# Performance work log

Measured on AMD Instinct MI355X. Metric: run time of the kernel, lower is better.

## Reference

```python
import jax, jax.numpy as jnp
import numpy as np

B, DV, W, H = 64, 2048, 14, 14
DQ, DA, G, DH, NC = 2400, 1200, 2, 1200, 3000


def setup_inputs() -> dict:
    key = jax.random.key(0)
    ks = jax.random.split(key, 14)
    s = lambda k, shp, scale=0.02: jax.random.normal(k, shp, dtype=jnp.float32) * scale
    return {
        "input_q": jax.random.normal(ks[0], (B, DQ), dtype=jnp.float32),
        "input_v": jax.random.normal(ks[1], (B, DV, W, H), dtype=jnp.float32),
        "Wv_att": s(ks[2], (DA, DV)),
        "bv_att": s(ks[3], (DA,)),
        "Wq_att": s(ks[4], (DA, DQ)),
        "bq_att": s(ks[5], (DA,)),
        "Watt": s(ks[6], (G, DA)),
        "batt": s(ks[7], (G,)),
        "Wv_fus": s(ks[8], (G, DH, DV)),
        "bv_fus": s(ks[9], (G, DH)),
        "Wq_fus": s(ks[10], (G * DH, DQ)),
        "bq_fus": s(ks[11], (G * DH,)),
        "Wc": s(ks[12], (NC, G * DH)),
        "bc": s(ks[13], (NC,)),
    }


def reference(input_q, input_v, Wv_att, bv_att, Wq_att, bq_att, Watt, batt,
              Wv_fus, bv_fus, Wq_fus, bq_fus, Wc, bc):
    b, dv, w, h = input_v.shape
    n = w * h  # spatial positions

    # --- attention branch (eval mode: dropout = identity) ---
    # 1x1 conv == per-position linear over channels; activation_v = tanh
    xv = jnp.tanh(jnp.einsum('bchw,dc->bdhw', input_v, Wv_att) + bv_att[None, :, None, None])
    xv = xv.reshape(b, -1, n).transpose(0, 2, 1)               # [B, WH, DA]
    # question projection; activation_q = tanh
    xq = jnp.tanh(input_q @ Wq_att.T + bq_att)                 # [B, DA]
    # MLB Hadamard fusion + activation_mm = tanh
    xatt = jnp.tanh(xv * xq[:, None, :])                       # [B, WH, DA]
    # glimpse scores: 1x1 conv over dim_mm channels
    wgt = jnp.einsum('bnd,gd->bgn', xatt, Watt) + batt[None, :, None]  # [B, G, WH]
    att = jax.nn.softmax(wgt, axis=-1)                         # softmax over WH per glimpse

    # weighted sum of ORIGINAL features per glimpse
    v_flat = input_v.reshape(b, dv, n)                         # [B, DV, WH]
    v_att = jnp.einsum('bgn,bdn->bgd', att, v_flat)            # [B, G, DV]

    # --- glimpse fusion + classification ---
    v_fus = jnp.tanh(jnp.einsum('bgd,ghd->bgh', v_att, Wv_fus) + bv_fus)  # [B, G, DH]
    v_fus = v_fus.reshape(b, -1)                               # [B, G*DH] (concat over glimpses)
    q_fus = jnp.tanh(input_q @ Wq_fus.T + bq_fus)              # [B, G*DH]
    x = (v_fus * q_fus) @ Wc.T + bc                            # [B, NC]
    return (x, wgt)
```

## Files before the change

kernel.cpp:

```cpp
#include <hip/hip_runtime.h>
#include <hip/hip_fp16.h>

typedef _Float16 half8 __attribute__((ext_vector_type(8)));
typedef float f32x4 __attribute__((ext_vector_type(4)));

__device__ __forceinline__ float tanh_fast(float x) {
  float e = __expf(2.0f * x);
  return 1.0f - 2.0f / (e + 1.0f);
}

__device__ __forceinline__ void gload16(const _Float16* g, _Float16* l) {
  __builtin_amdgcn_global_load_lds((const __attribute__((address_space(1))) void*)g,
                                   (__attribute__((address_space(3))) void*)l,
                                   16, 0, 0);
}

__global__ __launch_bounds__(256) void k_transpose_v(const float* __restrict__ in,
                                                     _Float16* __restrict__ out) {
  __shared__ float t[64][65];
  int b = blockIdx.z;
  int c0 = blockIdx.y * 64;
  int p0 = blockIdx.x * 64;
  int tid = threadIdx.x;
  int pl = tid & 63;
  #pragma unroll
  for (int s = 0; s < 16; ++s) {
    int cl = (tid >> 6) + s * 4;
    int p = p0 + pl;
    t[cl][pl] = (p < 196) ? in[((size_t)b * 2048 + (c0 + cl)) * 196 + p] : 0.0f;
  }
  __syncthreads();
  int c8 = (tid & 7) * 8;
  #pragma unroll
  for (int s = 0; s < 2; ++s) {
    int p = p0 + (tid >> 3) + s * 32;
    if (p < 196) {
      half8 v;
      #pragma unroll
      for (int j = 0; j < 8; ++j) v[j] = (_Float16)t[c8 + j][(tid >> 3) + s * 32];
      *(half8*)(out + ((size_t)b * 196 + p) * 2048 + c0 + c8) = v;
    }
  }
}

__global__ __launch_bounds__(256) void k_prep(const float* __restrict__ W,
                                              _Float16* __restrict__ Wh,
                                              const float* __restrict__ batt,
                                              float* __restrict__ wgt) {
  int i = blockIdx.x * 256 + threadIdx.x;
  int n = i >> 11;
  Wh[i] = (n < 1200) ? (_Float16)W[i] : (_Float16)0.0f;
  if (i < 25088) wgt[i] = batt[(i / 196) & 1];
}

__global__ __launch_bounds__(512, 2) void k_gemm1(const _Float16* __restrict__ A,
                                                  const _Float16* __restrict__ B,
                                                  const float* __restrict__ bias,
                                                  const float* __restrict__ xq,
                                                  const float* __restrict__ Watt,
                                                  float* __restrict__ wgt) {
  __shared__ __align__(16) _Float16 AS[2][256 * 64];
  __shared__ __align__(16) _Float16 BS[2][256 * 64];
  int tid = threadIdx.x;
  int lin = blockIdx.y * 5 + blockIdx.x;
  int xcd = lin & 7;
  int loc = lin >> 3;
  int nw = (xcd < 5 ? xcd * 31 : 155 + (xcd - 5) * 30) + loc;
  int n0 = (nw % 5) * 256;
  int m0 = (nw / 5) * 256;
  int lane = tid & 63;
  int wave = tid >> 6;
  int wm = (wave >> 2) * 128;
  int wn = (wave & 3) * 64;
  int fr = lane & 15;
  int fq = lane >> 4;

  int aIdx[2], bIdx[2];
  #pragma unroll
  for (int kk = 0; kk < 2; ++kk) {
    int sw = (((kk * 4 + fq) ^ (fr & 7)) << 3);
    aIdx[kk] = (wm + fr) * 64 + sw;
    bIdx[kk] = (wn + fr) * 64 + sw;
  }

  int lr = lane >> 3;
  int swz8 = ((lane & 7) ^ lr) << 3;
  const _Float16* aSrc[2][2];
  const _Float16* bSrc[2][2];
  int aDst[2][2], bDst[2][2];
  #pragma unroll
  for (int h = 0; h < 2; ++h)
    #pragma unroll
    for (int j = 0; j < 2; ++j) {
      int ra = j * 128 + h * 64 + wave * 8;
      aSrc[h][j] = A + (size_t)(m0 + ra + lr) * 2048 + swz8;
      aDst[h][j] = ra * 64;
      int rb = (j * 2 + (wave >> 2)) * 64 + h * 32 + (wave & 3) * 8;
      bSrc[h][j] = B + (size_t)(n0 + rb + lr) * 2048 + swz8;
      bDst[h][j] = rb * 64;
    }

  f32x4 acc[8][4];
  #pragma unroll
  for (int i = 0; i < 8; ++i)
    #pragma unroll
    for (int j = 0; j < 4; ++j) acc[i][j] = (f32x4){0.f, 0.f, 0.f, 0.f};

  auto stA = [&](int buf, int h, int off) {
    gload16(aSrc[h][0] + off, &AS[buf][aDst[h][0]]);
    gload16(aSrc[h][1] + off, &AS[buf][aDst[h][1]]);
  };
  auto stB = [&](int buf, int h, int off) {
    gload16(bSrc[h][0] + off, &BS[buf][bDst[h][0]]);
    gload16(bSrc[h][1] + off, &BS[buf][bDst[h][1]]);
  };
  auto dsA = [&](int buf, int mh, half8 (&a)[4][2]) {
    #pragma unroll
    for (int mt = 0; mt < 4; ++mt)
      #pragma unroll
      for (int kk = 0; kk < 2; ++kk)
        a[mt][kk] = *(const half8*)&AS[0][aIdx[kk] + (buf * 16384 + mh * 4096 + mt * 1024)];
  };
  auto dsB = [&](int buf, int nh, half8 (&b)[2][2]) {
    #pragma unroll
    for (int nt = 0; nt < 2; ++nt)
      #pragma unroll
      for (int kk = 0; kk < 2; ++kk)
        b[nt][kk] = *(const half8*)&BS[0][bIdx[kk] + (buf * 16384 + nh * 2048 + nt * 1024)];
  };
  auto mma = [&](half8 (&a)[4][2], half8 (&b)[2][2], int mh, int nh) {
    __builtin_amdgcn_s_setprio(1);
    #pragma unroll
    for (int kk = 0; kk < 2; ++kk)
      #pragma unroll
      for (int mt = 0; mt < 4; ++mt)
        #pragma unroll
        for (int nt = 0; nt < 2; ++nt)
          acc[mh * 4 + mt][nh * 2 + nt] = __builtin_amdgcn_mfma_f32_16x16x32_f16(
              a[mt][kk], b[nt][kk], acc[mh * 4 + mt][nh * 2 + nt], 0, 0, 0);
    __builtin_amdgcn_s_setprio(0);
  };

#define BAR() __builtin_amdgcn_s_barrier()
#define FENCE() asm volatile("" ::: "memory")
#define LGKM0() asm volatile("s_waitcnt lgkmcnt(0)")
#define LGKM8() asm volatile("s_waitcnt lgkmcnt(8)")

  stA(0, 0, 0); stB(0, 0, 0); stB(0, 1, 0); stA(0, 1, 0);
  stA(1, 0, 64); stB(1, 0, 64); stB(1, 1, 64);
  asm volatile("s_waitcnt vmcnt(6)" ::: "memory");
  BAR();
  FENCE();

  half8 a[4][2], b0[2][2], b1[2][2];
  for (int i = 0; i < 16; ++i) {
    const bool nl = (i < 15);
    dsA(0, 0, a); dsB(0, 0, b0);
    stA(1, 1, 64);
    LGKM8();
    BAR(); LGKM0();
    mma(a, b0, 0, 0);
    BAR();
    dsB(0, 1, b1);
    if (nl) stA(0, 0, 128);
    BAR(); LGKM0();
    mma(a, b1, 0, 1);
    BAR();
    dsA(0, 1, a);
    if (nl) stB(0, 0, 128);
    BAR(); LGKM0();
    mma(a, b1, 1, 1);
    BAR();
    if (nl) {
      stB(0, 1, 128);
      asm volatile("s_waitcnt vmcnt(6)" ::: "memory");
    } else {
      asm volatile("s_waitcnt vmcnt(0)" ::: "memory");
    }
    BAR();
    FENCE();
    mma(a, b0, 1, 0);
    BAR();
    dsA(1, 0, a); dsB(1, 0, b0);
    if (nl) stA(0, 1, 128);
    LGKM8();
    BAR(); LGKM0();
    mma(a, b0, 0, 0);
    BAR();
    dsB(1, 1, b1);
    if (nl) stA(1, 0, 192);
    BAR(); LGKM0();
    mma(a, b1, 0, 1);
    BAR();
    dsA(1, 1, a);
    if (nl) stB(1, 0, 192);
    BAR(); LGKM0();
    mma(a, b1, 1, 1);
    BAR();
    if (nl) {
      stB(1, 1, 192);
      asm volatile("s_waitcnt vmcnt(6)" ::: "memory");
    }
    BAR();
    FENCE();
    mma(a, b0, 1, 0);
    BAR();
    #pragma unroll
    for (int h = 0; h < 2; ++h)
      #pragma unroll
      for (int j = 0; j < 2; ++j) { aSrc[h][j] += 128; bSrc[h][j] += 128; }
  }
#undef BAR
#undef FENCE
#undef LGKM0
#undef LGKM8

  float bcol[4], wa0c[4], wa1c[4], xqv[4];
  int colv[4]; bool okv[4];
  #pragma unroll
  for (int nf = 0; nf < 4; ++nf) {
    int col = n0 + wn + (nf >> 1) * 32 + (nf & 1) * 16 + fr;
    bool ok = col < 1200;
    colv[nf] = col; okv[nf] = ok;
    bcol[nf] = ok ? bias[col] : 0.f;
    wa0c[nf] = ok ? Watt[col] : 0.f;
    wa1c[nf] = ok ? Watt[1200 + col] : 0.f;
    xqv[nf] = 0.f;
  }
  int bprev = -1;
  #pragma unroll
  for (int mf = 0; mf < 8; ++mf) {
    #pragma unroll
    for (int r = 0; r < 4; ++r) {
      int row = m0 + wm + (mf >> 2) * 64 + (mf & 3) * 16 + fq * 4 + r;
      int b = row / 196;
      if (b != bprev) {
        bprev = b;
        #pragma unroll
        for (int nf = 0; nf < 4; ++nf)
          xqv[nf] = okv[nf] ? xq[b * 1200 + colv[nf]] : 0.f;
      }
      float t0 = 0.f, t1 = 0.f;
      #pragma unroll
      for (int nf = 0; nf < 4; ++nf) {
        float xv = tanh_fast(acc[mf][nf][r] + bcol[nf]);
        float xa = tanh_fast(xv * xqv[nf]);
        t0 += xa * wa0c[nf];
        t1 += xa * wa1c[nf];
      }
      #pragma unroll
      for (int off = 8; off > 0; off >>= 1) {
        t0 += __shfl_down(t0, off);
        t1 += __shfl_down(t1, off);
      }
      if (fr == 0) {
        int p = row - b * 196;
        atomicAdd(&wgt[(b * 2 + 0) * 196 + p], t0);
        atomicAdd(&wgt[(b * 2 + 1) * 196 + p], t1);
      }
    }
  }
}

__global__ __launch_bounds__(512) void k_vatt(const _Float16* __restrict__ Vt,
                                              const float* __restrict__ wgt,
                                              float* __restrict__ v_att) {
  __shared__ float a0s[196], a1s[196];
  __shared__ float red[2][3][128][9];
  int b = blockIdx.y;
  int tid = threadIdx.x;
  int wv = tid >> 6, lane = tid & 63;
  if (wv < 2) {
    const float* wr = wgt + ((size_t)b * 2 + wv) * 196;
    float v[4];
    #pragma unroll
    for (int i = 0; i < 4; ++i) {
      int n = lane + i * 64;
      v[i] = (n < 196) ? wr[n] : -1e30f;
    }
    float mx = fmaxf(fmaxf(v[0], v[1]), fmaxf(v[2], v[3]));
    #pragma unroll
    for (int off = 32; off > 0; off >>= 1) mx = fmaxf(mx, __shfl_xor(mx, off));
    float s = 0.f;
    #pragma unroll
    for (int i = 0; i < 4; ++i) {
      int n = lane + i * 64;
      float e = (n < 196) ? __expf(v[i] - mx) : 0.f;
      v[i] = e;
      s += e;
    }
    #pragma unroll
    for (int off = 32; off > 0; off >>= 1) s += __shfl_xor(s, off);
    float inv = 1.f / s;
    float* dst = wv ? a1s : a0s;
    #pragma unroll
    for (int i = 0; i < 4; ++i) {
      int n = lane + i * 64;
      if (n < 196) dst[n] = v[i] * inv;
    }
  }
  __syncthreads();
  int nc = tid >> 7;
  int dl = tid & 127;
  int d = blockIdx.x * 1024 + dl * 8;
  const _Float16* vp = Vt + (size_t)b * 196 * 2048 + d;
  float s0[8] = {}, s1[8] = {};
  for (int n = nc * 49; n < nc * 49 + 49; ++n) {
    half8 v = *(const half8*)(vp + (size_t)n * 2048);
    float a0 = a0s[n], a1 = a1s[n];
    #pragma unroll
    for (int j = 0; j < 8; ++j) {
      float f = (float)v[j];
      s0[j] += a0 * f;
      s1[j] += a1 * f;
    }
  }
  if (nc > 0) {
    #pragma unroll
    for (int j = 0; j < 8; ++j) {
      red[0][nc - 1][dl][j] = s0[j];
      red[1][nc - 1][dl][j] = s1[j];
    }
  }
  __syncthreads();
  if (nc == 0) {
    #pragma unroll
    for (int c = 0; c < 3; ++c)
      #pragma unroll
      for (int j = 0; j < 8; ++j) {
        s0[j] += red[0][c][dl][j];
        s1[j] += red[1][c][dl][j];
      }
    #pragma unroll
    for (int j = 0; j < 8; ++j) {
      v_att[((size_t)b * 2 + 0) * 2048 + d + j] = s0[j];
      v_att[((size_t)b * 2 + 1) * 2048 + d + j] = s1[j];
    }
  }
}

__global__ __launch_bounds__(256) void k_skinnyQ(const float* __restrict__ q,
                                                 const float* __restrict__ Wa,
                                                 const float* __restrict__ Wf,
                                                 int S, float* __restrict__ P) {
  __shared__ __align__(16) float As[32][64];
  __shared__ __align__(16) float Ws2[32][64];
  int tid = threadIdx.x;
  int x = blockIdx.x;
  int s = blockIdx.y;
  bool f = x >= 19;
  const float* W = f ? Wf : Wa;
  int nt0 = f ? (x - 19) * 64 : x * 64;
  int N = f ? 2400 : 1200;
  int colBase = f ? 1200 : 0;
  const int K = 2400;
  int tiles = K >> 5;
  int t0 = (s * tiles) / S;
  int t1 = ((s + 1) * tiles) / S;
  int tx = tid & 15, ty = tid >> 4;
  int lm = tid >> 2;
  int lk = (tid & 3) * 8;
  const float* Ab = q + (size_t)lm * K;
  int ng = nt0 + lm;
  const float* Wb = W + (size_t)ng * K;
  bool wok = ng < N;
  float acc[4][4] = {};
  for (int t = t0; t < t1; ++t) {
    int k0 = t * 32;
    __syncthreads();
    #pragma unroll
    for (int j = 0; j < 8; ++j) As[lk + j][lm] = Ab[k0 + lk + j];
    #pragma unroll
    for (int j = 0; j < 8; ++j) Ws2[lk + j][lm] = wok ? Wb[k0 + lk + j] : 0.0f;
    __syncthreads();
    #pragma unroll
    for (int kk = 0; kk < 32; ++kk) {
      f32x4 a = *(const f32x4*)&As[kk][ty * 4];
      f32x4 wv = *(const f32x4*)&Ws2[kk][tx * 4];
      #pragma unroll
      for (int i = 0; i < 4; ++i)
        #pragma unroll
        for (int j = 0; j < 4; ++j) acc[i][j] += a[i] * wv[j];
    }
  }
  #pragma unroll
  for (int i = 0; i < 4; ++i) {
    int m = ty * 4 + i;
    #pragma unroll
    for (int j = 0; j < 4; ++j) {
      int nl = nt0 + tx * 4 + j;
      if (nl < N) P[((size_t)s * 64 + m) * 3600 + colBase + nl] = acc[i][j];
    }
  }
}

__global__ __launch_bounds__(256) void k_combineQ(const float* __restrict__ P, int S,
                                                  const float* __restrict__ bq_att,
                                                  const float* __restrict__ bq_fus,
                                                  float* __restrict__ xq,
                                                  float* __restrict__ q_fus) {
  int i = blockIdx.x * 256 + threadIdx.x;
  if (i >= 230400) return;
  int row = i / 3600, col = i % 3600;
  float sum = 0.f;
  for (int ss = 0; ss < S; ++ss) sum += P[(size_t)ss * 230400 + i];
  if (col < 1200) xq[row * 1200 + col] = tanh_fast(sum + bq_att[col]);
  else            q_fus[row * 2400 + col - 1200] = tanh_fast(sum + bq_fus[col - 1200]);
}

__global__ __launch_bounds__(256) void k_skinny(const float* __restrict__ A1,
                                                const float* __restrict__ A2,
                                                int lda, int strideAz,
                                                const float* __restrict__ W, long strideWz,
                                                int N, int K, int S,
                                                float* __restrict__ P, int ldp, int colOffZ) {
  __shared__ __align__(16) float As[32][64];
  __shared__ __align__(16) float Ws2[32][64];
  int tid = threadIdx.x;
  int z = blockIdx.z;
  int s = blockIdx.y;
  int nt0 = blockIdx.x * 64;
  int tiles = K >> 5;
  int t0 = (s * tiles) / S;
  int t1 = ((s + 1) * tiles) / S;
  int tx = tid & 15, ty = tid >> 4;
  int lm = tid >> 2;
  int lk = (tid & 3) * 8;
  const float* Ab = A1 + (size_t)z * strideAz + (size_t)lm * lda;
  const float* A2b = A2 ? (A2 + (size_t)z * strideAz + (size_t)lm * lda) : nullptr;
  int ng = nt0 + lm;
  const float* Wb = W + (size_t)z * strideWz + (size_t)ng * K;
  bool wok = ng < N;
  float acc[4][4] = {};
  for (int t = t0; t < t1; ++t) {
    int k0 = t * 32;
    __syncthreads();
    #pragma unroll
    for (int j = 0; j < 8; ++j) {
      float v = Ab[k0 + lk + j];
      if (A2b) v *= A2b[k0 + lk + j];
      As[lk + j][lm] = v;
    }
    #pragma unroll
    for (int j = 0; j < 8; ++j) Ws2[lk + j][lm] = wok ? Wb[k0 + lk + j] : 0.0f;
    __syncthreads();
    #pragma unroll
    for (int kk = 0; kk < 32; ++kk) {
      f32x4 a = *(const f32x4*)&As[kk][ty * 4];
      f32x4 wv = *(const f32x4*)&Ws2[kk][tx * 4];
      #pragma unroll
      for (int i = 0; i < 4; ++i)
        #pragma unroll
        for (int j = 0; j < 4; ++j) acc[i][j] += a[i] * wv[j];
    }
  }
  #pragma unroll
  for (int i = 0; i < 4; ++i) {
    int m = ty * 4 + i;
    #pragma unroll
    for (int j = 0; j < 4; ++j) {
      int nl = nt0 + tx * 4 + j;
      if (nl < N) P[((size_t)s * 64 + m) * ldp + z * colOffZ + nl] = acc[i][j];
    }
  }
}

__global__ __launch_bounds__(256) void k_combineVh(const float* __restrict__ P, int S,
                                                   const float* __restrict__ bv_fus,
                                                   const float* __restrict__ q_fus,
                                                   float* __restrict__ h) {
  int i = blockIdx.x * 256 + threadIdx.x;
  if (i >= 153600) return;
  int col = i % 2400;
  float sum = bv_fus[col];
  for (int ss = 0; ss < S; ++ss) sum += P[(size_t)ss * 153600 + i];
  h[i] = tanh_fast(sum) * q_fus[i];
}

__global__ __launch_bounds__(256) void k_combine(const float* __restrict__ P, int S, int ldp,
                                                 const float* __restrict__ bias,
                                                 float* __restrict__ out, int total) {
  int i = blockIdx.x * 256 + threadIdx.x;
  if (i >= total) return;
  float sum = bias[i % ldp];
  for (int ss = 0; ss < S; ++ss) sum += P[(size_t)ss * total + i];
  out[i] = sum;
}

extern "C" void kernel_launch(void* const* d_in, const int* in_sizes, int n_in,
                              void* d_out, int out_size, void* d_ws, size_t ws_size,
                              hipStream_t stream) {
  const float* input_q = (const float*)d_in[0];
  const float* input_v = (const float*)d_in[1];
  const float* Wv_att  = (const float*)d_in[2];
  const float* bv_att  = (const float*)d_in[3];
  const float* Wq_att  = (const float*)d_in[4];
  const float* bq_att  = (const float*)d_in[5];
  const float* Watt    = (const float*)d_in[6];
  const float* batt    = (const float*)d_in[7];
  const float* Wv_fus  = (const float*)d_in[8];
  const float* bv_fus  = (const float*)d_in[9];
  const float* Wq_fus  = (const float*)d_in[10];
  const float* bq_fus  = (const float*)d_in[11];
  const float* Wc      = (const float*)d_in[12];
  const float* bc      = (const float*)d_in[13];
  float* out = (float*)d_out;

  char* ws = (char*)d_ws;
  _Float16* Vt   = (_Float16*)ws; ws += 51380224;
  _Float16* Wh   = (_Float16*)ws; ws += 5242880;
  float* xq      = (float*)ws;    ws += 307200;
  float* v_att   = (float*)ws;    ws += 1048576;
  float* v_fus   = (float*)ws;    ws += 614400;
  float* q_fus   = (float*)ws;    ws += 614400;
  float* P       = (float*)ws;    ws += 14745600;

  float* x_out   = out;
  float* wgt_out = out + 192000;

  const int S = 16;

  k_transpose_v<<<dim3(4, 32, 64), dim3(256), 0, stream>>>(input_v, Vt);
  k_prep<<<dim3(10240), dim3(256), 0, stream>>>(Wv_att, Wh, batt, wgt_out);

  k_skinnyQ<<<dim3(57, S), dim3(256), 0, stream>>>(input_q, Wq_att, Wq_fus, S, P);
  k_combineQ<<<dim3(900), dim3(256), 0, stream>>>(P, S, bq_att, bq_fus, xq, q_fus);

  k_gemm1<<<dim3(5, 49), dim3(512), 0, stream>>>(Vt, Wh, bv_att, xq, Watt, wgt_out);

  k_vatt<<<dim3(2, 64), dim3(512), 0, stream>>>(Vt, wgt_out, v_att);

  k_skinny<<<dim3(19, S, 2), dim3(256), 0, stream>>>(v_att, nullptr, 4096, 2048,
                                                     Wv_fus, 1200L * 2048L, 1200, 2048, S, P, 2400, 1200);
  k_combineVh<<<dim3(600), dim3(256), 0, stream>>>(P, S, bv_fus, q_fus, v_fus);

  k_skinny<<<dim3(47, S, 1), dim3(256), 0, stream>>>(v_fus, nullptr, 2400, 0,
                                                     Wc, 0, 3000, 2400, S, P, 3000, 0);
  k_combine<<<dim3(750), dim3(256), 0, stream>>>(P, S, 3000, bc, x_out, 192000);
}
```

Baseline: 448.4 us.

## Drop explicit LDS waits in GEMM pipeline and repartition v_att kernel

The GEMM main loop loses its hand-placed lgkmcnt waits and about half its barriers, so the compiler inserts the LDS-read waits itself and MFMA work can overlap with LDS loads. The order of the LDS fragment loads is also swapped. Separately, the attention-weighted sum kernel now runs 256 threads per block over 8x64 blocks, each covering 256 channels with 8 spatial chunks instead of 4. This gives more blocks and more parallelism across spatial positions. With fewer barriers there is a risk of LDS buffer overwrite races if the remaining barriers no longer fully protect buffer reuse.

```diff
diff --git a/kernel.cpp b/kernel.cpp
--- a/kernel.cpp
+++ b/kernel.cpp
@@ -116,16 +116,16 @@
   };
   auto dsA = [&](int buf, int mh, half8 (&a)[4][2]) {
     #pragma unroll
-    for (int mt = 0; mt < 4; ++mt)
-      #pragma unroll
-      for (int kk = 0; kk < 2; ++kk)
+    for (int kk = 0; kk < 2; ++kk)
+      #pragma unroll
+      for (int mt = 0; mt < 4; ++mt)
         a[mt][kk] = *(const half8*)&AS[0][aIdx[kk] + (buf * 16384 + mh * 4096 + mt * 1024)];
   };
   auto dsB = [&](int buf, int nh, half8 (&b)[2][2]) {
     #pragma unroll
-    for (int nt = 0; nt < 2; ++nt)
-      #pragma unroll
-      for (int kk = 0; kk < 2; ++kk)
+    for (int kk = 0; kk < 2; ++kk)
+      #pragma unroll
+      for (int nt = 0; nt < 2; ++nt)
         b[nt][kk] = *(const half8*)&BS[0][bIdx[kk] + (buf * 16384 + nh * 2048 + nt * 1024)];
   };
   auto mma = [&](half8 (&a)[4][2], half8 (&b)[2][2], int mh, int nh) {
@@ -143,8 +143,6 @@
 
 #define BAR() __builtin_amdgcn_s_barrier()
 #define FENCE() asm volatile("" ::: "memory")
-#define LGKM0() asm volatile("s_waitcnt lgkmcnt(0)")
-#define LGKM8() asm volatile("s_waitcnt lgkmcnt(8)")
 
   stA(0, 0, 0); stB(0, 0, 0); stB(0, 1, 0); stA(0, 1, 0);
   stA(1, 0, 64); stB(1, 0, 64); stB(1, 1, 64);
@@ -155,56 +153,44 @@
   half8 a[4][2], b0[2][2], b1[2][2];
   for (int i = 0; i < 16; ++i) {
     const bool nl = (i < 15);
-    dsA(0, 0, a); dsB(0, 0, b0);
+    dsB(0, 0, b0); dsA(0, 0, a);
     stA(1, 1, 64);
-    LGKM8();
-    BAR(); LGKM0();
     mma(a, b0, 0, 0);
-    BAR();
+    BAR(); FENCE();
     dsB(0, 1, b1);
     if (nl) stA(0, 0, 128);
-    BAR(); LGKM0();
     mma(a, b1, 0, 1);
-    BAR();
+    BAR(); FENCE();
     dsA(0, 1, a);
     if (nl) stB(0, 0, 128);
-    BAR(); LGKM0();
     mma(a, b1, 1, 1);
-    BAR();
+    BAR(); FENCE();
     if (nl) {
       stB(0, 1, 128);
       asm volatile("s_waitcnt vmcnt(6)" ::: "memory");
     } else {
       asm volatile("s_waitcnt vmcnt(0)" ::: "memory");
     }
-    BAR();
-    FENCE();
     mma(a, b0, 1, 0);
-    BAR();
-    dsA(1, 0, a); dsB(1, 0, b0);
+    BAR(); FENCE();
+    dsB(1, 0, b0); dsA(1, 0, a);
     if (nl) stA(0, 1, 128);
-    LGKM8();
-    BAR(); LGKM0();
     mma(a, b0, 0, 0);
-    BAR();
+    BAR(); FENCE();
     dsB(1, 1, b1);
     if (nl) stA(1, 0, 192);
-    BAR(); LGKM0();
     mma(a, b1, 0, 1);
-    BAR();
+    BAR(); FENCE();
     dsA(1, 1, a);
     if (nl) stB(1, 0, 192);
-    BAR(); LGKM0();
     mma(a, b1, 1, 1);
-    BAR();
+    BAR(); FENCE();
     if (nl) {
       stB(1, 1, 192);
       asm volatile("s_waitcnt vmcnt(6)" ::: "memory");
     }
-    BAR();
-    FENCE();
     mma(a, b0, 1, 0);
-    BAR();
+    BAR(); FENCE();
     #pragma unroll
     for (int h = 0; h < 2; ++h)
       #pragma unroll
@@ -212,8 +198,6 @@
   }
 #undef BAR
 #undef FENCE
-#undef LGKM0
-#undef LGKM8
 
   float bcol[4], wa0c[4], wa1c[4], xqv[4];
   int colv[4]; bool okv[4];
@@ -262,11 +246,11 @@
   }
 }
 
-__global__ __launch_bounds__(512) void k_vatt(const _Float16* __restrict__ Vt,
+__global__ __launch_bounds__(256) void k_vatt(const _Float16* __restrict__ Vt,
                                               const float* __restrict__ wgt,
                                               float* __restrict__ v_att) {
   __shared__ float a0s[196], a1s[196];
-  __shared__ float red[2][3][128][9];
+  __shared__ float red[2][7][32][9];
   int b = blockIdx.y;
   int tid = threadIdx.x;
   int wv = tid >> 6, lane = tid & 63;
@@ -300,12 +284,13 @@
     }
   }
   __syncthreads();
-  int nc = tid >> 7;
-  int dl = tid & 127;
-  int d = blockIdx.x * 1024 + dl * 8;
+  int dg = tid & 31;
+  int nc = tid >> 5;
+  int d = blockIdx.x * 256 + dg * 8;
   const _Float16* vp = Vt + (size_t)b * 196 * 2048 + d;
+  int nA = (nc * 196) >> 3, nB = ((nc + 1) * 196) >> 3;
   float s0[8] = {}, s1[8] = {};
-  for (int n = nc * 49; n < nc * 49 + 49; ++n) {
+  for (int n = nA; n < nB; ++n) {
     half8 v = *(const half8*)(vp + (size_t)n * 2048);
     float a0 = a0s[n], a1 = a1s[n];
     #pragma unroll
@@ -318,18 +303,18 @@
   if (nc > 0) {
     #pragma unroll
     for (int j = 0; j < 8; ++j) {
-      red[0][nc - 1][dl][j] = s0[j];
-      red[1][nc - 1][dl][j] = s1[j];
+      red[0][nc - 1][dg][j] = s0[j];
+      red[1][nc - 1][dg][j] = s1[j];
     }
   }
   __syncthreads();
   if (nc == 0) {
     #pragma unroll
-    for (int c = 0; c < 3; ++c)
+    for (int c = 0; c < 7; ++c)
       #pragma unroll
       for (int j = 0; j < 8; ++j) {
-        s0[j] += red[0][c][dl][j];
-        s1[j] += red[1][c][dl][j];
+        s0[j] += red[0][c][dg][j];
+        s1[j] += red[1][c][dg][j];
       }
     #pragma unroll
     for (int j = 0; j < 8; ++j) {
@@ -528,7 +513,7 @@
 
   k_gemm1<<<dim3(5, 49), dim3(512), 0, stream>>>(Vt, Wh, bv_att, xq, Watt, wgt_out);
 
-  k_vatt<<<dim3(2, 64), dim3(512), 0, stream>>>(Vt, wgt_out, v_att);
+  k_vatt<<<dim3(8, 64), dim3(256), 0, stream>>>(Vt, wgt_out, v_att);
 
   k_skinny<<<dim3(19, S, 2), dim3(256), 0, stream>>>(v_att, nullptr, 4096, 2048,
                                                      Wv_fus, 1200L * 2048L, 1200, 2048, S, P, 2400, 1200);
```

New measurement: 437.2 us. 2.5% less time.
